# Kernel tuning notes

Measured on AMD Instinct MI355X. Metric: run time of the kernel, lower is better.

The kernel has to match this reference:

```python
import jax, jax.numpy as jnp
import numpy as np


def _hippo_scale_params(N, L):
    """Replicates HiPPOScale.__init__ for discretization='bilinear' (pure numpy)."""
    q = np.arange(N, dtype=np.float64)
    col, row = np.meshgrid(q, q)
    r = 2 * q + 1
    M = -(np.where(row >= col, r, 0) - np.diag(q))
    T = np.sqrt(np.diag(2 * q + 1))
    A = T @ M @ np.linalg.inv(T)          # (N, N)
    B = np.diag(T)                         # (N,)
    ts = np.arange(1, L + 1, dtype=np.float64)[:, None, None]  # (L,1,1)
    At = A[None] / ts                      # A / t, batched over t
    I = np.eye(N, dtype=np.float64)
    Mm = I[None] - 0.5 * At
    Nn = I[None] + 0.5 * At
    A_stacked = np.linalg.solve(Mm, Nn)                      # (L, N, N)
    Bt = B[None, :] / ts[:, 0, :]                             # (L, N)
    B_stacked = np.linalg.solve(Mm, Bt[..., None])[..., 0]    # (L, N)
    return A_stacked.astype(np.float32), B_stacked.astype(np.float32)


def setup_inputs() -> dict:
    N, L, Bsz = 64, 4096, 64
    key = jax.random.key(0)
    A_st, B_st = _hippo_scale_params(N, L)
    inputs = jax.random.normal(key, (L, Bsz), dtype=jnp.float32)
    return {
        "inputs": inputs,                       # (L, B)
        "A_stacked": jnp.asarray(A_st),         # (L, N, N)
        "B_stacked": jnp.asarray(B_st),         # (L, N)
    }


def reference(inputs, A_stacked, B_stacked):
    # u[t, b, :] = inputs[t, b] * B_stacked[t, :]   -> (L, B, N)
    u = inputs[..., None] * B_stacked[:, None, :]

    # x[t] = A[t] @ x[t-1] + u[t], x[-1] = 0  (time-varying linear recurrence).
    # The torch code computes this via a divide-and-conquer unroll; here we use
    # the equivalent parallel associative scan with elements (A, u) and
    # composition (A2@A1, A2@u1 + u2).
    def combine(e1, e2):
        a1, u1 = e1
        a2, u2 = e2
        a = jnp.matmul(a2, a1)                                  # (l, N, N)
        v = jnp.einsum('...ij,...bj->...bi', a2, u1) + u2       # (l, B, N)
        return (a, v)

    _, x = jax.lax.associative_scan(combine, (A_stacked, u))
    return x  # (L, B, N)
```

## Files before the change

### kernel.cpp

```cpp
#include <hip/hip_runtime.h>
#include <hip/hip_bf16.h>

#define TL 4096
#define NB 64
#define CH 8
#define CN 512
#define AS 72

typedef __attribute__((ext_vector_type(8))) short short8;
typedef __attribute__((ext_vector_type(4))) short short4v;
typedef __attribute__((ext_vector_type(4))) float floatx4;
typedef __attribute__((ext_vector_type(4))) unsigned int uint4v;

__device__ inline floatx4 mfma_bf16(short8 a, short8 b, floatx4 c) {
    return __builtin_amdgcn_mfma_f32_16x16x32_bf16(a, b, c, 0, 0, 0);
}
__device__ inline short bf16_rne(float x) {
    union { __hip_bfloat16 b; unsigned short s; } u;
    u.b = __float2bfloat16(x);
    return (short)u.s;
}
__device__ inline void split_bf16(float x, short& h, short& l) {
    h = bf16_rne(x);
    union { unsigned u; float f; } hv; hv.u = ((unsigned)(unsigned short)h) << 16;
    l = bf16_rne(x - hv.f);
}
__device__ inline void cvt_frag(float4 a, float4 b, short8& H, short8& L) {
    float v[8] = {a.x,a.y,a.z,a.w,b.x,b.y,b.z,b.w};
#pragma unroll
    for (int r = 0; r < 8; ++r) { short hh,ll; split_bf16(v[r],hh,ll); H[r]=hh; L[r]=ll; }
}
__device__ inline void unpack_frag(uint4v a, uint4v b, short8& H, short8& L) {
#pragma unroll
    for (int r = 0; r < 4; ++r) {
        H[r]   = (short)(a[r] >> 16); L[r]   = (short)(a[r] & 0xFFFFu);
        H[4+r] = (short)(b[r] >> 16); L[4+r] = (short)(b[r] & 0xFFFFu);
    }
}

__global__ __launch_bounds__(256, 2)
void hippo_phase1(const float* __restrict__ inp, const float* __restrict__ Ag,
                  const float* __restrict__ Bst,
                  unsigned* __restrict__ P32, float* __restrict__ VT)
{
    __shared__ short SBh[2][NB][AS], SBl[2][NB][AS];
    __shared__ short VBh[2][NB][AS], VBl[2][NB][AS];

    const int tid = threadIdx.x;
    const int c = blockIdx.x, t0 = c * CH;
    const int w = tid >> 6, lane = tid & 63;
    const int quad = lane >> 4, l15 = lane & 15;
    const int arow = 16*w + l15;
    const int wr0  = 16*w + 4*quad;

    float4 rA[2][2];
#pragma unroll
    for (int kc = 0; kc < 2; ++kc) {
        const float* p = Ag + (size_t)(t0+1)*4096 + (size_t)arow*64 + 32*kc + 8*quad;
        rA[kc][0] = *(const float4*)p;
        rA[kc][1] = *(const float4*)(p + 4);
    }
    float4 bnxt = *(const float4*)(Bst + (size_t)(t0+1)*64 + wr0);
    float inxt[4];
#pragma unroll
    for (int ni = 0; ni < 4; ++ni) inxt[ni] = inp[(size_t)(t0+1)*64 + l15 + 16*ni];

    floatx4 accS[4], accV[4];
    {
        const float* A0 = Ag + (size_t)t0 * 4096;
        float4 b0 = *(const float4*)(Bst + (size_t)t0*64 + wr0);
        float bc[4] = {b0.x,b0.y,b0.z,b0.w};
#pragma unroll
        for (int ni = 0; ni < 4; ++ni) {
            const float ii = inp[(size_t)t0*64 + l15 + 16*ni];
#pragma unroll
            for (int r = 0; r < 4; ++r) {
                accS[ni][r] = A0[(size_t)(wr0 + r)*64 + l15 + 16*ni];
                accV[ni][r] = bc[r] * ii;
            }
        }
    }
#pragma unroll
    for (int ni = 0; ni < 4; ++ni) {
        const int cc = l15 + 16*ni;
        short4v h4, l4;
#pragma unroll
        for (int r = 0; r < 4; ++r) { short hh,ll; split_bf16(accS[ni][r],hh,ll); h4[r]=hh; l4[r]=ll; }
        *(short4v*)&SBh[0][cc][wr0] = h4; *(short4v*)&SBl[0][cc][wr0] = l4;
#pragma unroll
        for (int r = 0; r < 4; ++r) { short hh,ll; split_bf16(accV[ni][r],hh,ll); h4[r]=hh; l4[r]=ll; }
        *(short4v*)&VBh[0][cc][wr0] = h4; *(short4v*)&VBl[0][cc][wr0] = l4;
    }
    __syncthreads();

    short8 aH[2], aL[2];
#pragma unroll
    for (int kc = 0; kc < 2; ++kc) cvt_frag(rA[kc][0], rA[kc][1], aH[kc], aL[kc]);

    int cur = 0;
    float4 bcur = bnxt;
    float icur[4];
#pragma unroll
    for (int ni = 0; ni < 4; ++ni) icur[ni] = inxt[ni];

    for (int s = 1; s < CH; ++s) {
        if (s + 1 < CH) {
            const int t1 = t0 + s + 1;
#pragma unroll
            for (int kc = 0; kc < 2; ++kc) {
                const float* p = Ag + (size_t)t1*4096 + (size_t)arow*64 + 32*kc + 8*quad;
                rA[kc][0] = *(const float4*)p;
                rA[kc][1] = *(const float4*)(p + 4);
            }
            bnxt = *(const float4*)(Bst + (size_t)t1*64 + wr0);
#pragma unroll
            for (int ni = 0; ni < 4; ++ni) inxt[ni] = inp[(size_t)t1*64 + l15 + 16*ni];
        }
        {
            float bc[4] = {bcur.x,bcur.y,bcur.z,bcur.w};
#pragma unroll
            for (int ni = 0; ni < 4; ++ni)
#pragma unroll
            for (int r = 0; r < 4; ++r) {
                accS[ni][r] = 0.0f;
                accV[ni][r] = bc[r] * icur[ni];
            }
        }
#pragma unroll
        for (int kc = 0; kc < 2; ++kc) {
            const int ko = 32*kc + 8*quad;
#pragma unroll
            for (int ni = 0; ni < 4; ++ni) {
                const int n = l15 + 16*ni;
                short8 sH = *(const short8*)&SBh[cur][n][ko];
                short8 sL = *(const short8*)&SBl[cur][n][ko];
                short8 vH = *(const short8*)&VBh[cur][n][ko];
                short8 vL = *(const short8*)&VBl[cur][n][ko];
                accS[ni] = mfma_bf16(aH[kc], sH, accS[ni]);
                accS[ni] = mfma_bf16(aH[kc], sL, accS[ni]);
                accS[ni] = mfma_bf16(aL[kc], sH, accS[ni]);
                accV[ni] = mfma_bf16(aH[kc], vH, accV[ni]);
                accV[ni] = mfma_bf16(aH[kc], vL, accV[ni]);
                accV[ni] = mfma_bf16(aL[kc], vH, accV[ni]);
            }
        }
        if (s + 1 < CH) {
#pragma unroll
            for (int kc = 0; kc < 2; ++kc) cvt_frag(rA[kc][0], rA[kc][1], aH[kc], aL[kc]);
            const int nb = cur ^ 1;
#pragma unroll
            for (int ni = 0; ni < 4; ++ni) {
                const int cc = l15 + 16*ni;
                short4v h4, l4;
#pragma unroll
                for (int r = 0; r < 4; ++r) { short hh,ll; split_bf16(accS[ni][r],hh,ll); h4[r]=hh; l4[r]=ll; }
                *(short4v*)&SBh[nb][cc][wr0] = h4; *(short4v*)&SBl[nb][cc][wr0] = l4;
#pragma unroll
                for (int r = 0; r < 4; ++r) { short hh,ll; split_bf16(accV[ni][r],hh,ll); h4[r]=hh; l4[r]=ll; }
                *(short4v*)&VBh[nb][cc][wr0] = h4; *(short4v*)&VBl[nb][cc][wr0] = l4;
            }
            __syncthreads();
            cur ^= 1;
        }
        bcur = bnxt;
#pragma unroll
        for (int ni = 0; ni < 4; ++ni) icur[ni] = inxt[ni];
    }

    unsigned* po = P32 + (size_t)c * 4096;
#pragma unroll
    for (int ni = 0; ni < 4; ++ni) {
        const int cc = l15 + 16*ni;
        *(floatx4*)(VT + (size_t)c*4096 + cc*64 + wr0) = accV[ni];
#pragma unroll
        for (int r = 0; r < 4; ++r) {
            short hh, ll; split_bf16(accS[ni][r], hh, ll);
            po[(size_t)(wr0 + r)*64 + cc] = ((unsigned)(unsigned short)hh << 16) | (unsigned)(unsigned short)ll;
        }
    }
}

__global__ __launch_bounds__(256, 2)
void hippo_seqscan(unsigned* __restrict__ P32, float* __restrict__ VT,
                   int bstride, int off0, int estride)
{
    __shared__ short PBh[2][NB][AS], PBl[2][NB][AS];
    __shared__ short VBh[2][NB][AS], VBl[2][NB][AS];

    const int tid = threadIdx.x;
    const int base = blockIdx.x * bstride + off0;
    const int w = tid >> 6, lane = tid & 63;
    const int quad = lane >> 4, l15 = lane & 15;
    const int arow = 16*w + l15;
    const int wr0  = 16*w + 4*quad;

    {
        const unsigned* p0 = P32 + (size_t)base * 4096;
        const float*    v0 = VT  + (size_t)base * 4096;
#pragma unroll
        for (int q = 0; q < 4; ++q) {
            int f = tid + q * 256;
            int k = f & 63, m0 = (f >> 6) * 4;
            uint4v pk = *(const uint4v*)(p0 + k * 64 + m0);
#pragma unroll
            for (int r = 0; r < 4; ++r) {
                PBh[0][m0 + r][k] = (short)(pk[r] >> 16);
                PBl[0][m0 + r][k] = (short)(pk[r] & 0xFFFFu);
            }
        }
#pragma unroll
        for (int q = 0; q < 4; ++q) {
            int f = tid + q * 256;
            int n = f >> 4, k0 = (f & 15) * 4;
            float4 vv = *(const float4*)(v0 + n * 64 + k0);
            float va[4] = {vv.x, vv.y, vv.z, vv.w};
            short4v vh4, vl4;
#pragma unroll
            for (int r = 0; r < 4; ++r) { short hh, ll; split_bf16(va[r], hh, ll); vh4[r]=hh; vl4[r]=ll; }
            *(short4v*)&VBh[0][n][k0] = vh4; *(short4v*)&VBl[0][n][k0] = vl4;
        }
    }
    uint4v rP[2][2]; float4 preV[4];
    {
        const unsigned* pc = P32 + (size_t)(base + estride) * 4096;
        const float*    vc = VT  + (size_t)(base + estride) * 4096;
#pragma unroll
        for (int kc = 0; kc < 2; ++kc) {
            const unsigned* p = pc + (size_t)arow*64 + 32*kc + 8*quad;
            rP[kc][0] = *(const uint4v*)p;
            rP[kc][1] = *(const uint4v*)(p + 4);
        }
#pragma unroll
        for (int ni = 0; ni < 4; ++ni)
            preV[ni] = *(const float4*)(vc + (size_t)(l15 + 16*ni)*64 + wr0);
    }
    __syncthreads();

    short8 aH[2], aL[2];
#pragma unroll
    for (int kc = 0; kc < 2; ++kc) unpack_frag(rP[kc][0], rP[kc][1], aH[kc], aL[kc]);

    int cur = 0;
    for (int i = 1; i < 8; ++i) {
        const int idx = base + i * estride;
        floatx4 accP[4], accV[4];
#pragma unroll
        for (int ni = 0; ni < 4; ++ni) {
            accV[ni][0] = preV[ni].x; accV[ni][1] = preV[ni].y;
            accV[ni][2] = preV[ni].z; accV[ni][3] = preV[ni].w;
            accP[ni][0]=accP[ni][1]=accP[ni][2]=accP[ni][3]=0.0f;
        }
        if (i + 1 < 8) {
            const unsigned* pc = P32 + (size_t)(base + (i+1) * estride) * 4096;
            const float*    vc = VT  + (size_t)(base + (i+1) * estride) * 4096;
#pragma unroll
            for (int kc = 0; kc < 2; ++kc) {
                const unsigned* p = pc + (size_t)arow*64 + 32*kc + 8*quad;
                rP[kc][0] = *(const uint4v*)p;
                rP[kc][1] = *(const uint4v*)(p + 4);
            }
#pragma unroll
            for (int ni = 0; ni < 4; ++ni)
                preV[ni] = *(const float4*)(vc + (size_t)(l15 + 16*ni)*64 + wr0);
        }
#pragma unroll
        for (int kc = 0; kc < 2; ++kc) {
            const int ko = 32*kc + 8*quad;
#pragma unroll
            for (int ni = 0; ni < 4; ++ni) {
                const int n = l15 + 16*ni;
                short8 pH = *(const short8*)&PBh[cur][n][ko];
                short8 pL = *(const short8*)&PBl[cur][n][ko];
                short8 vH = *(const short8*)&VBh[cur][n][ko];
                short8 vL = *(const short8*)&VBl[cur][n][ko];
                accP[ni] = mfma_bf16(aH[kc], pH, accP[ni]);
                accP[ni] = mfma_bf16(aH[kc], pL, accP[ni]);
                accP[ni] = mfma_bf16(aL[kc], pH, accP[ni]);
                accV[ni] = mfma_bf16(aH[kc], vH, accV[ni]);
                accV[ni] = mfma_bf16(aH[kc], vL, accV[ni]);
                accV[ni] = mfma_bf16(aL[kc], vH, accV[ni]);
            }
        }
        if (i + 1 < 8) {
#pragma unroll
            for (int kc = 0; kc < 2; ++kc) unpack_frag(rP[kc][0], rP[kc][1], aH[kc], aL[kc]);
        }
        unsigned* po = P32 + (size_t)idx * 4096;
        const int nb = cur ^ 1;
#pragma unroll
        for (int ni = 0; ni < 4; ++ni) {
            const int cc = l15 + 16*ni;
            *(floatx4*)(VT + (size_t)idx*4096 + cc*64 + wr0) = accV[ni];
            short4v h4, l4;
#pragma unroll
            for (int r = 0; r < 4; ++r) {
                short hh, ll; split_bf16(accP[ni][r], hh, ll);
                po[(size_t)(wr0+r)*64 + cc] = ((unsigned)(unsigned short)hh << 16) | (unsigned)(unsigned short)ll;
                h4[r]=hh; l4[r]=ll;
            }
            if (i + 1 < 8) {
                *(short4v*)&PBh[nb][cc][wr0] = h4; *(short4v*)&PBl[nb][cc][wr0] = l4;
                short4v vh4, vl4;
#pragma unroll
                for (int r = 0; r < 4; ++r) { short hh,ll; split_bf16(accV[ni][r],hh,ll); vh4[r]=hh; vl4[r]=ll; }
                *(short4v*)&VBh[nb][cc][wr0] = vh4; *(short4v*)&VBl[nb][cc][wr0] = vl4;
            }
        }
        if (i + 1 < 8) __syncthreads();
        cur ^= 1;
    }
}

__global__ __launch_bounds__(256, 2)
void hippo_s3(unsigned* __restrict__ P32, const float* __restrict__ VT)
{
    __shared__ short EBh[2][NB][AS], EBl[2][NB][AS];
    const int tid = threadIdx.x;
    const int w = tid >> 6, lane = tid & 63, quad = lane >> 4, l15 = lane & 15;
    const int arow = 16*w + l15;
    const int wr0  = 16*w + 4*quad;

#pragma unroll
    for (int q = 0; q < 16; ++q) {
        int f = tid + q * 256; EBh[0][f >> 6][f & 63] = 0; EBl[0][f >> 6][f & 63] = 0;
    }
    uint4v rP[2][2]; float4 preV[4];
    {
        const unsigned* pc = P32 + (size_t)63 * 4096;
        const float*    vc = VT  + (size_t)63 * 4096;
#pragma unroll
        for (int kc = 0; kc < 2; ++kc) {
            const unsigned* p = pc + (size_t)arow*64 + 32*kc + 8*quad;
            rP[kc][0] = *(const uint4v*)p;
            rP[kc][1] = *(const uint4v*)(p + 4);
        }
#pragma unroll
        for (int ni = 0; ni < 4; ++ni)
            preV[ni] = *(const float4*)(vc + (size_t)(l15 + 16*ni)*64 + wr0);
    }
    __syncthreads();

    short8 aH[2], aL[2];
#pragma unroll
    for (int kc = 0; kc < 2; ++kc) unpack_frag(rP[kc][0], rP[kc][1], aH[kc], aL[kc]);

    int cur = 0;
    for (int s = 0; s < 7; ++s) {
        const int idx = 64 * s + 63;
        floatx4 acc[4];
#pragma unroll
        for (int ni = 0; ni < 4; ++ni) {
            acc[ni][0] = preV[ni].x; acc[ni][1] = preV[ni].y;
            acc[ni][2] = preV[ni].z; acc[ni][3] = preV[ni].w;
        }
        if (s + 1 < 7) {
            const int idx2 = 64 * (s + 1) + 63;
            const unsigned* pc = P32 + (size_t)idx2 * 4096;
            const float*    vc = VT  + (size_t)idx2 * 4096;
#pragma unroll
            for (int kc = 0; kc < 2; ++kc) {
                const unsigned* p = pc + (size_t)arow*64 + 32*kc + 8*quad;
                rP[kc][0] = *(const uint4v*)p;
                rP[kc][1] = *(const uint4v*)(p + 4);
            }
#pragma unroll
            for (int ni = 0; ni < 4; ++ni)
                preV[ni] = *(const float4*)(vc + (size_t)(l15 + 16*ni)*64 + wr0);
        }
#pragma unroll
        for (int kc = 0; kc < 2; ++kc) {
            const int ko = 32*kc + 8*quad;
#pragma unroll
            for (int ni = 0; ni < 4; ++ni) {
                const int n = l15 + 16*ni;
                short8 eH = *(const short8*)&EBh[cur][n][ko];
                short8 eL = *(const short8*)&EBl[cur][n][ko];
                acc[ni] = mfma_bf16(aH[kc], eH, acc[ni]);
                acc[ni] = mfma_bf16(aH[kc], eL, acc[ni]);
                acc[ni] = mfma_bf16(aL[kc], eH, acc[ni]);
            }
        }
        if (s + 1 < 7) {
#pragma unroll
            for (int kc = 0; kc < 2; ++kc) unpack_frag(rP[kc][0], rP[kc][1], aH[kc], aL[kc]);
        }
        float* eo = (float*)(P32 + (size_t)idx * 4096);
        const int nb = cur ^ 1;
#pragma unroll
        for (int ni = 0; ni < 4; ++ni) {
            const int cc = l15 + 16*ni;
            *(floatx4*)(eo + cc*64 + wr0) = acc[ni];
            if (s + 1 < 7) {
                short4v h4, l4;
#pragma unroll
                for (int r = 0; r < 4; ++r) { short hh,ll; split_bf16(acc[ni][r],hh,ll); h4[r]=hh; l4[r]=ll; }
                *(short4v*)&EBh[nb][cc][wr0] = h4; *(short4v*)&EBl[nb][cc][wr0] = l4;
            }
        }
        if (s + 1 < 7) __syncthreads();
        cur ^= 1;
    }
}

__global__ __launch_bounds__(256, 2)
void hippo_phase3(const float* __restrict__ inp, const float* __restrict__ Ag,
                  const float* __restrict__ Bst, const unsigned* __restrict__ P32,
                  const float* __restrict__ VT, float* __restrict__ out)
{
    __shared__ short XBh[2][NB][AS], XBl[2][NB][AS];

    const int tid = threadIdx.x, c = blockIdx.x, t0 = c * CH;
    const int w = tid >> 6, lane = tid & 63, quad = lane >> 4, l15 = lane & 15;
    const int arow = 16*w + l15;
    const int wr0  = 16*w + 4*quad;
    const int sup = c >> 6, g = c >> 3, gi = g & 7, j = c & 7;

    float4 rA[2][2];
#pragma unroll
    for (int kc = 0; kc < 2; ++kc) {
        const float* p = Ag + (size_t)t0*4096 + (size_t)arow*64 + 32*kc + 8*quad;
        rA[kc][0] = *(const float4*)p;
        rA[kc][1] = *(const float4*)(p + 4);
    }
    float4 bcur = *(const float4*)(Bst + (size_t)t0*64 + wr0);
    float icur[4];
#pragma unroll
    for (int ni = 0; ni < 4; ++ni) icur[ni] = inp[(size_t)t0*64 + l15 + 16*ni];

    if (sup == 0) {
#pragma unroll
        for (int q = 0; q < 16; ++q) { int f = tid + q*256; XBh[0][f>>6][f&63] = 0; XBl[0][f>>6][f&63] = 0; }
    } else {
        const float* e = (const float*)(P32 + (size_t)(64*(sup-1) + 63) * 4096);
#pragma unroll
        for (int q = 0; q < 4; ++q) {
            int f = tid + q*256; int b = f>>4, k0 = (f&15)*4;
            float4 v = *(const float4*)(e + b*64 + k0);
            float va[4] = {v.x,v.y,v.z,v.w};
            short4v h4, l4;
#pragma unroll
            for (int r=0;r<4;++r){short hh,ll;split_bf16(va[r],hh,ll);h4[r]=hh;l4[r]=ll;}
            *(short4v*)&XBh[0][b][k0] = h4; *(short4v*)&XBl[0][b][k0] = l4;
        }
    }
    __syncthreads();
    int cur = 0;

    auto combine = [&](int idx) {
        uint4v rP[2][2];
        const unsigned* pc = P32 + (size_t)idx * 4096;
        const float*    vc = VT  + (size_t)idx * 4096;
#pragma unroll
        for (int kc = 0; kc < 2; ++kc) {
            const unsigned* p = pc + (size_t)arow*64 + 32*kc + 8*quad;
            rP[kc][0] = *(const uint4v*)p;
            rP[kc][1] = *(const uint4v*)(p + 4);
        }
        floatx4 acc[4];
#pragma unroll
        for (int ni = 0; ni < 4; ++ni) {
            float4 vv = *(const float4*)(vc + (size_t)(l15 + 16*ni)*64 + wr0);
            acc[ni][0]=vv.x; acc[ni][1]=vv.y; acc[ni][2]=vv.z; acc[ni][3]=vv.w;
        }
        short8 cH[2], cL[2];
#pragma unroll
        for (int kc = 0; kc < 2; ++kc) unpack_frag(rP[kc][0], rP[kc][1], cH[kc], cL[kc]);
#pragma unroll
        for (int kc = 0; kc < 2; ++kc) {
            const int ko = 32*kc + 8*quad;
#pragma unroll
            for (int ni = 0; ni < 4; ++ni) {
                const int n = l15 + 16*ni;
                short8 xH = *(const short8*)&XBh[cur][n][ko];
                short8 xL = *(const short8*)&XBl[cur][n][ko];
                acc[ni] = mfma_bf16(cH[kc], xH, acc[ni]);
                acc[ni] = mfma_bf16(cH[kc], xL, acc[ni]);
                acc[ni] = mfma_bf16(cL[kc], xH, acc[ni]);
            }
        }
        const int nb = cur ^ 1;
#pragma unroll
        for (int ni = 0; ni < 4; ++ni) {
            const int cc = l15 + 16*ni;
            short4v h4, l4;
#pragma unroll
            for (int r=0;r<4;++r){short hh,ll;split_bf16(acc[ni][r],hh,ll);h4[r]=hh;l4[r]=ll;}
            *(short4v*)&XBh[nb][cc][wr0] = h4; *(short4v*)&XBl[nb][cc][wr0] = l4;
        }
        __syncthreads();
        cur ^= 1;
    };
    if (gi) combine(8*g - 1);
    if (j)  combine(c - 1);

    short8 aH[2], aL[2];
#pragma unroll
    for (int kc = 0; kc < 2; ++kc) cvt_frag(rA[kc][0], rA[kc][1], aH[kc], aL[kc]);

    float4 bnxt; float inxt[4];
    floatx4 acc[4];
    for (int s = 0; s < CH; ++s) {
        const int t = t0 + s;
        if (s + 1 < CH) {
            const int t1 = t + 1;
#pragma unroll
            for (int kc = 0; kc < 2; ++kc) {
                const float* p = Ag + (size_t)t1*4096 + (size_t)arow*64 + 32*kc + 8*quad;
                rA[kc][0] = *(const float4*)p;
                rA[kc][1] = *(const float4*)(p + 4);
            }
            bnxt = *(const float4*)(Bst + (size_t)t1*64 + wr0);
#pragma unroll
            for (int ni = 0; ni < 4; ++ni) inxt[ni] = inp[(size_t)t1*64 + l15 + 16*ni];
        }
        {
            float bc[4] = {bcur.x,bcur.y,bcur.z,bcur.w};
#pragma unroll
            for (int ni=0;ni<4;++ni)
#pragma unroll
            for (int r=0;r<4;++r) acc[ni][r] = bc[r] * icur[ni];
        }
#pragma unroll
        for (int kc = 0; kc < 2; ++kc) {
            const int ko = 32*kc + 8*quad;
#pragma unroll
            for (int ni = 0; ni < 4; ++ni) {
                const int n = l15 + 16*ni;
                short8 xH = *(const short8*)&XBh[cur][n][ko];
                short8 xL = *(const short8*)&XBl[cur][n][ko];
                acc[ni] = mfma_bf16(aH[kc], xH, acc[ni]);
                acc[ni] = mfma_bf16(aH[kc], xL, acc[ni]);
                acc[ni] = mfma_bf16(aL[kc], xH, acc[ni]);
            }
        }
        if (s + 1 < CH) {
#pragma unroll
            for (int kc = 0; kc < 2; ++kc) cvt_frag(rA[kc][0], rA[kc][1], aH[kc], aL[kc]);
        }
        const int nb = cur ^ 1;
#pragma unroll
        for (int ni = 0; ni < 4; ++ni) {
            const int cc = l15 + 16*ni;
            *(floatx4*)(out + (size_t)t*4096 + cc*64 + wr0) = acc[ni];
            if (s + 1 < CH) {
                short4v h4, l4;
#pragma unroll
                for (int r=0;r<4;++r){short hh,ll;split_bf16(acc[ni][r],hh,ll);h4[r]=hh;l4[r]=ll;}
                *(short4v*)&XBh[nb][cc][wr0] = h4; *(short4v*)&XBl[nb][cc][wr0] = l4;
            }
        }
        if (s + 1 < CH) { __syncthreads(); cur ^= 1; }
        bcur = bnxt;
#pragma unroll
        for (int ni = 0; ni < 4; ++ni) icur[ni] = inxt[ni];
    }
}

extern "C" void kernel_launch(void* const* d_in, const int* in_sizes, int n_in,
                              void* d_out, int out_size, void* d_ws, size_t ws_size,
                              hipStream_t stream)
{
    const float* inp = (const float*)d_in[0];
    const float* A   = (const float*)d_in[1];
    const float* Bst = (const float*)d_in[2];
    float* out = (float*)d_out;
    float* ws  = (float*)d_ws;

    unsigned* P32 = (unsigned*)ws;
    float*    VT  = ws + (size_t)CN * 4096;

    hippo_phase1<<<CN, 256, 0, stream>>>(inp, A, Bst, P32, VT);
    hippo_seqscan<<<64, 256, 0, stream>>>(P32, VT, 8, 0, 1);
    hippo_seqscan<<<8, 256, 0, stream>>>(P32, VT, 64, 7, 8);
    hippo_s3<<<1, 256, 0, stream>>>(P32, VT);
    hippo_phase3<<<CN, 256, 0, stream>>>(inp, A, Bst, P32, VT, out);
}
```

Measured before the change: 183.9 us.

## Fuse three scan-level kernels into one with global atomic barriers

Merges the two seqscan launches and the single-block s3 launch into one 64-block kernel. Blocks signal completion through global atomic counters, and the surviving blocks spin-wait before running the next level. This removes two kernel-launch boundaries and their drain/ramp gaps on the sequential critical path. In exchange it adds a memset of the counters and relies on all 64 blocks being co-resident to avoid deadlock.

```diff
diff --git a/kernel.cpp b/kernel.cpp
--- a/kernel.cpp
+++ b/kernel.cpp
@@ -181,78 +181,49 @@
 }
 
 __global__ __launch_bounds__(256, 2)
-void hippo_seqscan(unsigned* __restrict__ P32, float* __restrict__ VT,
-                   int bstride, int off0, int estride)
+void hippo_scan(unsigned* __restrict__ P32, float* __restrict__ VT,
+                unsigned* __restrict__ gbar)
 {
     __shared__ short PBh[2][NB][AS], PBl[2][NB][AS];
     __shared__ short VBh[2][NB][AS], VBl[2][NB][AS];
 
-    const int tid = threadIdx.x;
-    const int base = blockIdx.x * bstride + off0;
+    const int tid = threadIdx.x, c = blockIdx.x;
     const int w = tid >> 6, lane = tid & 63;
     const int quad = lane >> 4, l15 = lane & 15;
     const int arow = 16*w + l15;
     const int wr0  = 16*w + 4*quad;
 
-    {
-        const unsigned* p0 = P32 + (size_t)base * 4096;
-        const float*    v0 = VT  + (size_t)base * 4096;
-#pragma unroll
-        for (int q = 0; q < 4; ++q) {
-            int f = tid + q * 256;
-            int k = f & 63, m0 = (f >> 6) * 4;
-            uint4v pk = *(const uint4v*)(p0 + k * 64 + m0);
-#pragma unroll
-            for (int r = 0; r < 4; ++r) {
-                PBh[0][m0 + r][k] = (short)(pk[r] >> 16);
-                PBl[0][m0 + r][k] = (short)(pk[r] & 0xFFFFu);
-            }
-        }
-#pragma unroll
-        for (int q = 0; q < 4; ++q) {
-            int f = tid + q * 256;
-            int n = f >> 4, k0 = (f & 15) * 4;
-            float4 vv = *(const float4*)(v0 + n * 64 + k0);
-            float va[4] = {vv.x, vv.y, vv.z, vv.w};
-            short4v vh4, vl4;
-#pragma unroll
-            for (int r = 0; r < 4; ++r) { short hh, ll; split_bf16(va[r], hh, ll); vh4[r]=hh; vl4[r]=ll; }
-            *(short4v*)&VBh[0][n][k0] = vh4; *(short4v*)&VBl[0][n][k0] = vl4;
-        }
-    }
-    uint4v rP[2][2]; float4 preV[4];
-    {
-        const unsigned* pc = P32 + (size_t)(base + estride) * 4096;
-        const float*    vc = VT  + (size_t)(base + estride) * 4096;
-#pragma unroll
-        for (int kc = 0; kc < 2; ++kc) {
-            const unsigned* p = pc + (size_t)arow*64 + 32*kc + 8*quad;
-            rP[kc][0] = *(const uint4v*)p;
-            rP[kc][1] = *(const uint4v*)(p + 4);
-        }
-#pragma unroll
-        for (int ni = 0; ni < 4; ++ni)
-            preV[ni] = *(const float4*)(vc + (size_t)(l15 + 16*ni)*64 + wr0);
-    }
-    __syncthreads();
-
-    short8 aH[2], aL[2];
-#pragma unroll
-    for (int kc = 0; kc < 2; ++kc) unpack_frag(rP[kc][0], rP[kc][1], aH[kc], aL[kc]);
-
-    int cur = 0;
-    for (int i = 1; i < 8; ++i) {
-        const int idx = base + i * estride;
-        floatx4 accP[4], accV[4];
-#pragma unroll
-        for (int ni = 0; ni < 4; ++ni) {
-            accV[ni][0] = preV[ni].x; accV[ni][1] = preV[ni].y;
-            accV[ni][2] = preV[ni].z; accV[ni][3] = preV[ni].w;
-            accP[ni][0]=accP[ni][1]=accP[ni][2]=accP[ni][3]=0.0f;
-        }
-        if (i + 1 < 8) {
-            const unsigned* pc = P32 + (size_t)(base + (i+1) * estride) * 4096;
-            const float*    vc = VT  + (size_t)(base + (i+1) * estride) * 4096;
+    auto scan8 = [&](int base, int estride) {
+        {
+            const unsigned* p0 = P32 + (size_t)base * 4096;
+            const float*    v0 = VT  + (size_t)base * 4096;
+#pragma unroll
+            for (int q = 0; q < 4; ++q) {
+                int f = tid + q * 256;
+                int k = f & 63, m0 = (f >> 6) * 4;
+                uint4v pk = *(const uint4v*)(p0 + k * 64 + m0);
+#pragma unroll
+                for (int r = 0; r < 4; ++r) {
+                    PBh[0][m0 + r][k] = (short)(pk[r] >> 16);
+                    PBl[0][m0 + r][k] = (short)(pk[r] & 0xFFFFu);
+                }
+            }
+#pragma unroll
+            for (int q = 0; q < 4; ++q) {
+                int f = tid + q * 256;
+                int n = f >> 4, k0 = (f & 15) * 4;
+                float4 vv = *(const float4*)(v0 + n * 64 + k0);
+                float va[4] = {vv.x, vv.y, vv.z, vv.w};
+                short4v vh4, vl4;
+#pragma unroll
+                for (int r = 0; r < 4; ++r) { short hh, ll; split_bf16(va[r], hh, ll); vh4[r]=hh; vl4[r]=ll; }
+                *(short4v*)&VBh[0][n][k0] = vh4; *(short4v*)&VBl[0][n][k0] = vl4;
+            }
+        }
+        uint4v rP[2][2]; float4 pV[4];
+        {
+            const unsigned* pc = P32 + (size_t)(base + estride) * 4096;
+            const float*    vc = VT  + (size_t)(base + estride) * 4096;
 #pragma unroll
             for (int kc = 0; kc < 2; ++kc) {
                 const unsigned* p = pc + (size_t)arow*64 + 32*kc + 8*quad;
@@ -261,102 +232,126 @@
             }
 #pragma unroll
             for (int ni = 0; ni < 4; ++ni)
-                preV[ni] = *(const float4*)(vc + (size_t)(l15 + 16*ni)*64 + wr0);
-        }
-#pragma unroll
-        for (int kc = 0; kc < 2; ++kc) {
-            const int ko = 32*kc + 8*quad;
-#pragma unroll
-            for (int ni = 0; ni < 4; ++ni) {
-                const int n = l15 + 16*ni;
-                short8 pH = *(const short8*)&PBh[cur][n][ko];
-                short8 pL = *(const short8*)&PBl[cur][n][ko];
-                short8 vH = *(const short8*)&VBh[cur][n][ko];
-                short8 vL = *(const short8*)&VBl[cur][n][ko];
-                accP[ni] = mfma_bf16(aH[kc], pH, accP[ni]);
-                accP[ni] = mfma_bf16(aH[kc], pL, accP[ni]);
-                accP[ni] = mfma_bf16(aL[kc], pH, accP[ni]);
-                accV[ni] = mfma_bf16(aH[kc], vH, accV[ni]);
-                accV[ni] = mfma_bf16(aH[kc], vL, accV[ni]);
-                accV[ni] = mfma_bf16(aL[kc], vH, accV[ni]);
-            }
-        }
-        if (i + 1 < 8) {
-#pragma unroll
-            for (int kc = 0; kc < 2; ++kc) unpack_frag(rP[kc][0], rP[kc][1], aH[kc], aL[kc]);
-        }
-        unsigned* po = P32 + (size_t)idx * 4096;
-        const int nb = cur ^ 1;
-#pragma unroll
-        for (int ni = 0; ni < 4; ++ni) {
-            const int cc = l15 + 16*ni;
-            *(floatx4*)(VT + (size_t)idx*4096 + cc*64 + wr0) = accV[ni];
-            short4v h4, l4;
-#pragma unroll
-            for (int r = 0; r < 4; ++r) {
-                short hh, ll; split_bf16(accP[ni][r], hh, ll);
-                po[(size_t)(wr0+r)*64 + cc] = ((unsigned)(unsigned short)hh << 16) | (unsigned)(unsigned short)ll;
-                h4[r]=hh; l4[r]=ll;
+                pV[ni] = *(const float4*)(vc + (size_t)(l15 + 16*ni)*64 + wr0);
+        }
+        __syncthreads();
+
+        short8 aH[2], aL[2];
+#pragma unroll
+        for (int kc = 0; kc < 2; ++kc) unpack_frag(rP[kc][0], rP[kc][1], aH[kc], aL[kc]);
+
+        int cur = 0;
+        for (int i = 1; i < 8; ++i) {
+            const int idx = base + i * estride;
+            floatx4 accP[4], accV[4];
+#pragma unroll
+            for (int ni = 0; ni < 4; ++ni) {
+                accV[ni][0] = pV[ni].x; accV[ni][1] = pV[ni].y;
+                accV[ni][2] = pV[ni].z; accV[ni][3] = pV[ni].w;
+                accP[ni][0]=accP[ni][1]=accP[ni][2]=accP[ni][3]=0.0f;
             }
             if (i + 1 < 8) {
-                *(short4v*)&PBh[nb][cc][wr0] = h4; *(short4v*)&PBl[nb][cc][wr0] = l4;
-                short4v vh4, vl4;
-#pragma unroll
-                for (int r = 0; r < 4; ++r) { short hh,ll; split_bf16(accV[ni][r],hh,ll); vh4[r]=hh; vl4[r]=ll; }
-                *(short4v*)&VBh[nb][cc][wr0] = vh4; *(short4v*)&VBl[nb][cc][wr0] = vl4;
-            }
-        }
-        if (i + 1 < 8) __syncthreads();
-        cur ^= 1;
-    }
-}
-
-__global__ __launch_bounds__(256, 2)
-void hippo_s3(unsigned* __restrict__ P32, const float* __restrict__ VT)
-{
-    __shared__ short EBh[2][NB][AS], EBl[2][NB][AS];
-    const int tid = threadIdx.x;
-    const int w = tid >> 6, lane = tid & 63, quad = lane >> 4, l15 = lane & 15;
-    const int arow = 16*w + l15;
-    const int wr0  = 16*w + 4*quad;
-
-#pragma unroll
-    for (int q = 0; q < 16; ++q) {
-        int f = tid + q * 256; EBh[0][f >> 6][f & 63] = 0; EBl[0][f >> 6][f & 63] = 0;
-    }
-    uint4v rP[2][2]; float4 preV[4];
+                const unsigned* pc = P32 + (size_t)(base + (i+1) * estride) * 4096;
+                const float*    vc = VT  + (size_t)(base + (i+1) * estride) * 4096;
+#pragma unroll
+                for (int kc = 0; kc < 2; ++kc) {
+                    const unsigned* p = pc + (size_t)arow*64 + 32*kc + 8*quad;
+                    rP[kc][0] = *(const uint4v*)p;
+                    rP[kc][1] = *(const uint4v*)(p + 4);
+                }
+#pragma unroll
+                for (int ni = 0; ni < 4; ++ni)
+                    pV[ni] = *(const float4*)(vc + (size_t)(l15 + 16*ni)*64 + wr0);
+            }
+#pragma unroll
+            for (int kc = 0; kc < 2; ++kc) {
+                const int ko = 32*kc + 8*quad;
+#pragma unroll
+                for (int ni = 0; ni < 4; ++ni) {
+                    const int n = l15 + 16*ni;
+                    short8 pH = *(const short8*)&PBh[cur][n][ko];
+                    short8 pL = *(const short8*)&PBl[cur][n][ko];
+                    short8 vH = *(const short8*)&VBh[cur][n][ko];
+                    short8 vL = *(const short8*)&VBl[cur][n][ko];
+                    accP[ni] = mfma_bf16(aH[kc], pH, accP[ni]);
+                    accP[ni] = mfma_bf16(aH[kc], pL, accP[ni]);
+                    accP[ni] = mfma_bf16(aL[kc], pH, accP[ni]);
+                    accV[ni] = mfma_bf16(aH[kc], vH, accV[ni]);
+                    accV[ni] = mfma_bf16(aH[kc], vL, accV[ni]);
+                    accV[ni] = mfma_bf16(aL[kc], vH, accV[ni]);
+                }
+            }
+            if (i + 1 < 8) {
+#pragma unroll
+                for (int kc = 0; kc < 2; ++kc) unpack_frag(rP[kc][0], rP[kc][1], aH[kc], aL[kc]);
+            }
+            unsigned* po = P32 + (size_t)idx * 4096;
+            const int nb = cur ^ 1;
+#pragma unroll
+            for (int ni = 0; ni < 4; ++ni) {
+                const int cc = l15 + 16*ni;
+                *(floatx4*)(VT + (size_t)idx*4096 + cc*64 + wr0) = accV[ni];
+                short4v h4, l4;
+#pragma unroll
+                for (int r = 0; r < 4; ++r) {
+                    short hh, ll; split_bf16(accP[ni][r], hh, ll);
+                    po[(size_t)(wr0+r)*64 + cc] = ((unsigned)(unsigned short)hh << 16) | (unsigned)(unsigned short)ll;
+                    h4[r]=hh; l4[r]=ll;
+                }
+                if (i + 1 < 8) {
+                    *(short4v*)&PBh[nb][cc][wr0] = h4; *(short4v*)&PBl[nb][cc][wr0] = l4;
+                    short4v vh4, vl4;
+#pragma unroll
+                    for (int r = 0; r < 4; ++r) { short hh,ll; split_bf16(accV[ni][r],hh,ll); vh4[r]=hh; vl4[r]=ll; }
+                    *(short4v*)&VBh[nb][cc][wr0] = vh4; *(short4v*)&VBl[nb][cc][wr0] = vl4;
+                }
+            }
+            if (i + 1 < 8) __syncthreads();
+            cur ^= 1;
+        }
+    };
+
+    scan8(c * 8, 1);
+
+    __syncthreads();
+    if (tid == 0)
+        __hip_atomic_fetch_add(gbar + 0, 1u, __ATOMIC_RELEASE, __HIP_MEMORY_SCOPE_AGENT);
+    if (c >= 8) return;
+    if (tid == 0) {
+        unsigned v;
+        do {
+            __builtin_amdgcn_s_sleep(8);
+            v = __hip_atomic_load(gbar + 0, __ATOMIC_RELAXED, __HIP_MEMORY_SCOPE_AGENT);
+        } while (v < 64u);
+        (void)__hip_atomic_load(gbar + 0, __ATOMIC_ACQUIRE, __HIP_MEMORY_SCOPE_AGENT);
+    }
+    __syncthreads();
+
+    scan8(64 * c + 7, 8);
+
+    __syncthreads();
+    if (tid == 0)
+        __hip_atomic_fetch_add(gbar + 1, 1u, __ATOMIC_RELEASE, __HIP_MEMORY_SCOPE_AGENT);
+    if (c != 0) return;
+    if (tid == 0) {
+        unsigned v;
+        do {
+            __builtin_amdgcn_s_sleep(8);
+            v = __hip_atomic_load(gbar + 1, __ATOMIC_RELAXED, __HIP_MEMORY_SCOPE_AGENT);
+        } while (v < 8u);
+        (void)__hip_atomic_load(gbar + 1, __ATOMIC_ACQUIRE, __HIP_MEMORY_SCOPE_AGENT);
+    }
+    __syncthreads();
+
     {
-        const unsigned* pc = P32 + (size_t)63 * 4096;
-        const float*    vc = VT  + (size_t)63 * 4096;
-#pragma unroll
-        for (int kc = 0; kc < 2; ++kc) {
-            const unsigned* p = pc + (size_t)arow*64 + 32*kc + 8*quad;
-            rP[kc][0] = *(const uint4v*)p;
-            rP[kc][1] = *(const uint4v*)(p + 4);
-        }
-#pragma unroll
-        for (int ni = 0; ni < 4; ++ni)
-            preV[ni] = *(const float4*)(vc + (size_t)(l15 + 16*ni)*64 + wr0);
-    }
-    __syncthreads();
-
-    short8 aH[2], aL[2];
-#pragma unroll
-    for (int kc = 0; kc < 2; ++kc) unpack_frag(rP[kc][0], rP[kc][1], aH[kc], aL[kc]);
-
-    int cur = 0;
-    for (int s = 0; s < 7; ++s) {
-        const int idx = 64 * s + 63;
-        floatx4 acc[4];
-#pragma unroll
-        for (int ni = 0; ni < 4; ++ni) {
-            acc[ni][0] = preV[ni].x; acc[ni][1] = preV[ni].y;
-            acc[ni][2] = preV[ni].z; acc[ni][3] = preV[ni].w;
-        }
-        if (s + 1 < 7) {
-            const int idx2 = 64 * (s + 1) + 63;
-            const unsigned* pc = P32 + (size_t)idx2 * 4096;
-            const float*    vc = VT  + (size_t)idx2 * 4096;
+#pragma unroll
+        for (int q = 0; q < 16; ++q) {
+            int f = tid + q * 256; PBh[0][f >> 6][f & 63] = 0; PBl[0][f >> 6][f & 63] = 0;
+        }
+        uint4v rP[2][2]; float4 pV[4];
+        {
+            const unsigned* pc = P32 + (size_t)63 * 4096;
+            const float*    vc = VT  + (size_t)63 * 4096;
 #pragma unroll
             for (int kc = 0; kc < 2; ++kc) {
                 const unsigned* p = pc + (size_t)arow*64 + 32*kc + 8*quad;
@@ -365,40 +360,70 @@
             }
 #pragma unroll
             for (int ni = 0; ni < 4; ++ni)
-                preV[ni] = *(const float4*)(vc + (size_t)(l15 + 16*ni)*64 + wr0);
-        }
-#pragma unroll
-        for (int kc = 0; kc < 2; ++kc) {
-            const int ko = 32*kc + 8*quad;
-#pragma unroll
-            for (int ni = 0; ni < 4; ++ni) {
-                const int n = l15 + 16*ni;
-                short8 eH = *(const short8*)&EBh[cur][n][ko];
-                short8 eL = *(const short8*)&EBl[cur][n][ko];
-                acc[ni] = mfma_bf16(aH[kc], eH, acc[ni]);
-                acc[ni] = mfma_bf16(aH[kc], eL, acc[ni]);
-                acc[ni] = mfma_bf16(aL[kc], eH, acc[ni]);
-            }
-        }
-        if (s + 1 < 7) {
-#pragma unroll
-            for (int kc = 0; kc < 2; ++kc) unpack_frag(rP[kc][0], rP[kc][1], aH[kc], aL[kc]);
-        }
-        float* eo = (float*)(P32 + (size_t)idx * 4096);
-        const int nb = cur ^ 1;
-#pragma unroll
-        for (int ni = 0; ni < 4; ++ni) {
-            const int cc = l15 + 16*ni;
-            *(floatx4*)(eo + cc*64 + wr0) = acc[ni];
+                pV[ni] = *(const float4*)(vc + (size_t)(l15 + 16*ni)*64 + wr0);
+        }
+        __syncthreads();
+
+        short8 aH[2], aL[2];
+#pragma unroll
+        for (int kc = 0; kc < 2; ++kc) unpack_frag(rP[kc][0], rP[kc][1], aH[kc], aL[kc]);
+
+        int cur = 0;
+        for (int s = 0; s < 7; ++s) {
+            const int idx = 64 * s + 63;
+            floatx4 acc[4];
+#pragma unroll
+            for (int ni = 0; ni < 4; ++ni) {
+                acc[ni][0] = pV[ni].x; acc[ni][1] = pV[ni].y;
+                acc[ni][2] = pV[ni].z; acc[ni][3] = pV[ni].w;
+            }
             if (s + 1 < 7) {
-                short4v h4, l4;
-#pragma unroll
-                for (int r = 0; r < 4; ++r) { short hh,ll; split_bf16(acc[ni][r],hh,ll); h4[r]=hh; l4[r]=ll; }
-                *(short4v*)&EBh[nb][cc][wr0] = h4; *(short4v*)&EBl[nb][cc][wr0] = l4;
-            }
-        }
-        if (s + 1 < 7) __syncthreads();
-        cur ^= 1;
+                const int idx2 = 64 * (s + 1) + 63;
+                const unsigned* pc = P32 + (size_t)idx2 * 4096;
+                const float*    vc = VT  + (size_t)idx2 * 4096;
+#pragma unroll
+                for (int kc = 0; kc < 2; ++kc) {
+                    const unsigned* p = pc + (size_t)arow*64 + 32*kc + 8*quad;
+                    rP[kc][0] = *(const uint4v*)p;
+                    rP[kc][1] = *(const uint4v*)(p + 4);
+                }
+#pragma unroll
+                for (int ni = 0; ni < 4; ++ni)
+                    pV[ni] = *(const float4*)(vc + (size_t)(l15 + 16*ni)*64 + wr0);
+            }
+#pragma unroll
+            for (int kc = 0; kc < 2; ++kc) {
+                const int ko = 32*kc + 8*quad;
+#pragma unroll
+                for (int ni = 0; ni < 4; ++ni) {
+                    const int n = l15 + 16*ni;
+                    short8 eH = *(const short8*)&PBh[cur][n][ko];
+                    short8 eL = *(const short8*)&PBl[cur][n][ko];
+                    acc[ni] = mfma_bf16(aH[kc], eH, acc[ni]);
+                    acc[ni] = mfma_bf16(aH[kc], eL, acc[ni]);
+                    acc[ni] = mfma_bf16(aL[kc], eH, acc[ni]);
+                }
+            }
+            if (s + 1 < 7) {
+#pragma unroll
+                for (int kc = 0; kc < 2; ++kc) unpack_frag(rP[kc][0], rP[kc][1], aH[kc], aL[kc]);
+            }
+            float* eo = (float*)(P32 + (size_t)idx * 4096);
+            const int nb = cur ^ 1;
+#pragma unroll
+            for (int ni = 0; ni < 4; ++ni) {
+                const int cc = l15 + 16*ni;
+                *(floatx4*)(eo + cc*64 + wr0) = acc[ni];
+                if (s + 1 < 7) {
+                    short4v h4, l4;
+#pragma unroll
+                    for (int r = 0; r < 4; ++r) { short hh,ll; split_bf16(acc[ni][r],hh,ll); h4[r]=hh; l4[r]=ll; }
+                    *(short4v*)&PBh[nb][cc][wr0] = h4; *(short4v*)&PBl[nb][cc][wr0] = l4;
+                }
+            }
+            if (s + 1 < 7) __syncthreads();
+            cur ^= 1;
+        }
     }
 }
 
@@ -567,11 +592,11 @@
     float* ws  = (float*)d_ws;
 
     unsigned* P32 = (unsigned*)ws;
-    float*    VT  = ws + (size_t)CN * 4096;
-
+    float*    VT  = (float*)ws + (size_t)CN * 4096;
+    unsigned* gbar = (unsigned*)((char*)d_ws + (size_t)16 * 1024 * 1024);
+
+    hipMemsetAsync(gbar, 0, 2 * sizeof(unsigned), stream);
     hippo_phase1<<<CN, 256, 0, stream>>>(inp, A, Bst, P32, VT);
-    hippo_seqscan<<<64, 256, 0, stream>>>(P32, VT, 8, 0, 1);
-    hippo_seqscan<<<8, 256, 0, stream>>>(P32, VT, 64, 7, 8);
-    hippo_s3<<<1, 256, 0, stream>>>(P32, VT);
+    hippo_scan<<<64, 256, 0, stream>>>(P32, VT, gbar);
     hippo_phase3<<<CN, 256, 0, stream>>>(inp, A, Bst, P32, VT, out);
 }
```

After: 187.6 us. 2.0% more time.
